# Kernel tuning notes

Measured on AMD Instinct MI355X. Metric: run time of the kernel, lower is better.

The kernel has to match this reference:

```python
import jax, jax.numpy as jnp
import numpy as np

NUM_HEADS = 16
NUM_BUCKETS = 32
MAX_DISTANCE = 128


def _relative_position_bucket(relative_position, num_buckets=NUM_BUCKETS, max_distance=MAX_DISTANCE):
    # bidirectional=True (encoder self-attention)
    nb = num_buckets // 2  # 16
    buckets = (relative_position > 0).astype(jnp.int32) * nb
    rp = jnp.abs(relative_position)
    max_exact = nb // 2  # 8
    is_small = rp < max_exact
    # log-spaced bins for large distances; clamp arg of log to >=1 to avoid log(0)
    rp_f = jnp.maximum(rp, 1).astype(jnp.float32)
    large = max_exact + (
        jnp.log(rp_f / max_exact) / np.log(max_distance / max_exact) * (nb - max_exact)
    ).astype(jnp.int32)
    large = jnp.minimum(large, nb - 1)
    return buckets + jnp.where(is_small, rp, large)


def setup_inputs() -> dict:
    key = jax.random.key(0)
    ks = jax.random.split(key, 6)
    B, L, D = 2, 2048, 1024
    scale = 0.02  # keep activations in a sane range
    return {
        "hidden_states": jax.random.normal(ks[0], (B, L, D), dtype=jnp.float32),
        "Wq": jax.random.normal(ks[1], (D, D), dtype=jnp.float32) * scale,
        "Wk": jax.random.normal(ks[2], (D, D), dtype=jnp.float32) * scale,
        "Wv": jax.random.normal(ks[3], (D, D), dtype=jnp.float32) * scale,
        "Wo": jax.random.normal(ks[4], (D, D), dtype=jnp.float32) * scale,
        "bias_table": jax.random.normal(ks[5], (NUM_BUCKETS, NUM_HEADS), dtype=jnp.float32),
    }


def reference(hidden_states, Wq, Wk, Wv, Wo, bias_table):
    B, L, D = hidden_states.shape
    H = NUM_HEADS
    hd = D // H

    # projections (nn.Linear: y = x @ W.T), split heads -> [B, H, L, hd]
    def proj(x, W):
        return (x @ W.T).reshape(B, L, H, hd).transpose(0, 2, 1, 3)

    q = proj(hidden_states, Wq)
    k = proj(hidden_states, Wk)
    v = proj(hidden_states, Wv)

    # T5 relative position bias: [1, H, L, L]
    ctx = jnp.arange(L)[:, None]
    mem = jnp.arange(L)[None, :]
    buckets = _relative_position_bucket(mem - ctx)  # [L, L]
    position_bias = bias_table[buckets].transpose(2, 0, 1)[None]  # [1, H, L, L]

    # NOTE: T5-style attention has NO 1/sqrt(hd) scaling
    scores = jnp.einsum("bhqd,bhkd->bhqk", q, k) + position_bias
    attn = jax.nn.softmax(scores.astype(jnp.float32), axis=-1).astype(scores.dtype)
    out = jnp.einsum("bhqk,bhkd->bhqd", attn, v)
    out = out.transpose(0, 2, 1, 3).reshape(B, L, D)
    out = out @ Wo.T
    return out, position_bias
```

## Files before the change

kernel.cpp:

```cpp
#include <hip/hip_runtime.h>
#include <cstdint>
#include <cmath>

typedef unsigned short ushort_t;
typedef __bf16 bf16x8 __attribute__((ext_vector_type(8)));
typedef float f32x4 __attribute__((ext_vector_type(4)));
typedef ushort_t us4 __attribute__((ext_vector_type(4)));
typedef ushort_t us8 __attribute__((ext_vector_type(8)));

#define MFMA16(a, b, c) __builtin_amdgcn_mfma_f32_16x16x32_bf16(a, b, c, 0, 0, 0)
#define LOG2E 1.4426950408889634f

__device__ __forceinline__ ushort_t f2bf(float f) {
    uint32_t u = __float_as_uint(f);
    u = u + 0x7fffu + ((u >> 16) & 1u);
    return (ushort_t)(u >> 16);
}

__device__ __forceinline__ void glds16(const ushort_t* g, ushort_t* s) {
    __builtin_amdgcn_global_load_lds(
        (const __attribute__((address_space(1))) void*)(g),
        (__attribute__((address_space(3))) void*)(s), 16, 0, 0);
}

__global__ void cast_all_k(const float* __restrict__ x, const float* __restrict__ wq,
                           const float* __restrict__ wk, const float* __restrict__ wv,
                           const float* __restrict__ wo, ushort_t* __restrict__ xb,
                           ushort_t* __restrict__ wb) {
    int id = blockIdx.x, t = threadIdx.x;
    const float* src;
    ushort_t* dst;
    int idx;
    float scale = 1.0f;
    if (id < 4096) {
        src = x; dst = xb; idx = id * 256 + t;
    } else {
        int r = (id - 4096) >> 10;
        idx = ((id - 4096) & 1023) * 256 + t;
        src = (r == 0) ? wq : (r == 1) ? wk : (r == 2) ? wv : wo;
        dst = wb + (size_t)r * 1048576;
        if (r == 0) scale = LOG2E;
    }
    float4 v = ((const float4*)src)[idx];
    us4 o;
    o.x = f2bf(v.x * scale); o.y = f2bf(v.y * scale);
    o.z = f2bf(v.z * scale); o.w = f2bf(v.w * scale);
    ((us4*)dst)[idx] = o;
}

__global__ void make_lut_k(unsigned char* __restrict__ lut) {
    int idx = blockIdx.x * 256 + threadIdx.x;
    if (idx >= 4095) return;
    int rel = idx - 2047;
    int b = (rel > 0) ? 16 : 0;
    int rp = (rel < 0) ? -rel : rel;
    int add;
    if (rp < 8) {
        add = rp;
    } else {
        float lg = (float)::log((double)rp * 0.125);
        double t = ((double)lg) / 2.772588722239781 * 8.0;
        int large = 8 + (int)t;
        add = (large < 15) ? large : 15;
    }
    lut[idx] = (unsigned char)(b + add);
}

__global__ void write_bias_k(const unsigned char* __restrict__ lut, const float* __restrict__ table,
                             float* __restrict__ out2) {
    int t = blockIdx.x * 256 + threadIdx.x;
    int j4 = t & 511;
    int i = (t >> 9) & 2047;
    int h = t >> 20;
    int base = j4 * 4 - i + 2047;
    float4 v;
    v.x = table[lut[base + 0] * 16 + h];
    v.y = table[lut[base + 1] * 16 + h];
    v.z = table[lut[base + 2] * 16 + h];
    v.w = table[lut[base + 3] * 16 + h];
    ((float4*)out2)[t] = v;
}

template <int MODE>
__global__ __launch_bounds__(256) void gemm_bt_k(const ushort_t* __restrict__ A,
                                                 const ushort_t* __restrict__ B0,
                                                 void* __restrict__ C0,
                                                 int M, int N, int K, long sB, long sC) {
    __shared__ ushort_t As[128 * 64];
    __shared__ ushort_t Bs[128 * 64];
    const int tid = threadIdx.x;
    const int l = tid & 63, w = tid >> 6;
    const int quad = l >> 4, lc = l & 15;
    const int wm = w >> 1, wn = w & 1;
    const int m0 = blockIdx.y * 128, n0 = blockIdx.x * 128;
    const ushort_t* B = B0 + (long)blockIdx.z * sB;

    f32x4 acc[4][4] = {};
    const int rA = l >> 3;
    const int cA = ((l & 7) ^ rA) * 8;

    for (int k0 = 0; k0 < K; k0 += 64) {
#pragma unroll
        for (int t = 0; t < 4; ++t) {
            int row = w * 32 + t * 8;
            glds16(A + (size_t)(m0 + row + rA) * K + k0 + cA, &As[row * 64]);
            glds16(B + (size_t)(n0 + row + rA) * K + k0 + cA, &Bs[row * 64]);
        }
        __syncthreads();
#pragma unroll
        for (int ko = 0; ko < 2; ++ko) {
            const int ch = (((ko * 4 + quad) ^ (lc & 7))) * 8;
            bf16x8 af[4], bfr[4];
#pragma unroll
            for (int mt = 0; mt < 4; ++mt)
                af[mt] = *(const bf16x8*)&As[(wm * 64 + mt * 16 + lc) * 64 + ch];
#pragma unroll
            for (int nt = 0; nt < 4; ++nt)
                bfr[nt] = *(const bf16x8*)&Bs[(wn * 64 + nt * 16 + lc) * 64 + ch];
#pragma unroll
            for (int mt = 0; mt < 4; ++mt)
#pragma unroll
                for (int nt = 0; nt < 4; ++nt)
                    acc[mt][nt] = MFMA16(af[mt], bfr[nt], acc[mt][nt]);
        }
        __syncthreads();
    }
#pragma unroll
    for (int mt = 0; mt < 4; ++mt) {
#pragma unroll
        for (int nt = 0; nt < 4; ++nt) {
            int col = n0 + wn * 64 + nt * 16 + lc;
#pragma unroll
            for (int r = 0; r < 4; ++r) {
                int row = m0 + wm * 64 + mt * 16 + quad * 4 + r;
                if constexpr (MODE == 1) {
                    ((float*)C0)[(size_t)row * N + col] = acc[mt][nt][r];
                } else if constexpr (MODE == 0) {
                    (((ushort_t*)C0) + (long)blockIdx.z * sC)[(size_t)row * N + col] = f2bf(acc[mt][nt][r]);
                } else {
                    ((ushort_t*)C0)[(size_t)(col >> 11) * 2097152 + (size_t)row * 2048 + (col & 2047)] =
                        f2bf(acc[mt][nt][r]);
                }
            }
        }
    }
}

__global__ __launch_bounds__(256, 2) void attn_k(const ushort_t* __restrict__ Qg,
                                                 const ushort_t* __restrict__ Kg,
                                                 const ushort_t* __restrict__ VTg,
                                                 ushort_t* __restrict__ Ctx,
                                                 const unsigned char* __restrict__ lut,
                                                 const float* __restrict__ table) {
    __shared__ ushort_t Ks[128 * 64];
    __shared__ ushort_t VTs[64 * 128];
    __shared__ ushort_t QP[128 * 64];
    __shared__ float biasb[256];

    const int tid = threadIdx.x, l = tid & 63, w = tid >> 6;
    const int quad = l >> 4, lc = l & 15;
    const int id = blockIdx.x;
    const int bh = id & 31, b = bh >> 4, h = bh & 15;
    const int q0 = (id >> 5) * 128;
    const size_t tokbase = (size_t)b * 2048;

    const int rK = l >> 3;
    const int cK = ((l & 7) ^ rK) * 8;
    const int rV = l >> 4;
    const int cVi = l & 15;

#pragma unroll
    for (int t = 0; t < 4; ++t) {
        int row0 = w * 32 + t * 8;
        glds16(Qg + (tokbase + q0 + row0 + rK) * 1024 + h * 64 + cK, &QP[row0 * 64]);
        glds16(Kg + (tokbase + row0 + rK) * 1024 + h * 64 + cK, &Ks[row0 * 64]);
    }
#pragma unroll
    for (int t = 0; t < 4; ++t) {
        int row0 = w * 16 + t * 4;
        int rsw = ((t & 1) * 4 + rV) & 7;
        int csw = (cVi & 8) | ((cVi & 7) ^ rsw);
        glds16(VTg + (size_t)(b * 1024 + h * 64 + row0 + rV) * 2048 + csw * 8, &VTs[row0 * 128]);
    }
    if (tid < 255) biasb[tid] = table[(int)lut[0 - q0 + tid + 1920] * 16 + h] * LOG2E;
    __syncthreads();

    bf16x8 qf[2][2];
#pragma unroll
    for (int nt = 0; nt < 2; ++nt)
#pragma unroll
        for (int ko = 0; ko < 2; ++ko) {
            int row = w * 32 + nt * 16 + lc;
            int ch = ((ko * 4 + quad) ^ (lc & 7)) * 8;
            qf[nt][ko] = *(const bf16x8*)&QP[row * 64 + ch];
        }
    __syncthreads();

    float mstate[2] = {-1e30f, -1e30f};
    float lstate[2] = {0.f, 0.f};
    f32x4 acco[4][2] = {};
    ushort_t* Pw = &QP[w * 1280];
    const int cb0 = quad * 4 - (w * 32 + lc) + 127;
    const int cxor = lc & 3;

    for (int kt = 0; kt < 16; ++kt) {
        const int j0 = kt * 128;
        f32x4 accs[8][2] = {};
#pragma unroll
        for (int ko = 0; ko < 2; ++ko) {
            const int ch = ((ko * 4 + quad) ^ (lc & 7)) * 8;
#pragma unroll
            for (int mt = 0; mt < 8; ++mt) {
                bf16x8 kf = *(const bf16x8*)&Ks[(mt * 16 + lc) * 64 + ch];
                accs[mt][0] = MFMA16(kf, qf[0][ko], accs[mt][0]);
                accs[mt][1] = MFMA16(kf, qf[1][ko], accs[mt][1]);
            }
        }
        f32x4 bv[9];
#pragma unroll
        for (int d = 0; d < 9; ++d)
#pragma unroll
            for (int r = 0; r < 4; ++r) bv[d][r] = biasb[cb0 + (d - 1) * 16 + r];
#pragma unroll
        for (int mt = 0; mt < 8; ++mt)
#pragma unroll
            for (int nt = 0; nt < 2; ++nt)
                accs[mt][nt] += bv[mt - nt + 1];
#pragma unroll
        for (int nt = 0; nt < 2; ++nt) {
            float mx = accs[0][nt][0];
#pragma unroll
            for (int mt = 0; mt < 8; ++mt)
#pragma unroll
                for (int r = 0; r < 4; ++r) mx = fmaxf(mx, accs[mt][nt][r]);
            mx = fmaxf(mx, __shfl_xor(mx, 16, 64));
            mx = fmaxf(mx, __shfl_xor(mx, 32, 64));
            float mo = mstate[nt], mn = fmaxf(mo, mx);
            float alpha = exp2f(mo - mn);
            mstate[nt] = mn;
            float rs = 0.f;
#pragma unroll
            for (int mt = 0; mt < 8; ++mt)
#pragma unroll
                for (int r = 0; r < 4; ++r) {
                    float p = exp2f(accs[mt][nt][r] - mn);
                    accs[mt][nt][r] = p;
                    rs += p;
                }
            rs += __shfl_xor(rs, 16, 64);
            rs += __shfl_xor(rs, 32, 64);
            lstate[nt] = lstate[nt] * alpha + rs;
#pragma unroll
            for (int dt = 0; dt < 4; ++dt) acco[dt][nt] *= alpha;
        }
#pragma unroll
        for (int kk = 0; kk < 4; ++kk) {
#pragma unroll
            for (int half = 0; half < 2; ++half) {
                int mt = kk * 2 + half;
                int c = half * 2 + (quad >> 1);
                int coff = ((c ^ cxor) * 8 + (quad & 1) * 4);
#pragma unroll
                for (int nt = 0; nt < 2; ++nt) {
                    us4 o;
#pragma unroll
                    for (int r = 0; r < 4; ++r) o[r] = f2bf(accs[mt][nt][r]);
                    *(us4*)&Pw[(nt * 16 + lc) * 40 + coff] = o;
                }
            }
            bf16x8 pf[2];
#pragma unroll
            for (int nt = 0; nt < 2; ++nt)
                pf[nt] = *(const bf16x8*)&Pw[(nt * 16 + lc) * 40 + (quad ^ cxor) * 8];
            bf16x8 vf[4];
#pragma unroll
            for (int dt = 0; dt < 4; ++dt) {
                int ch = kk * 4 + quad;
                int chs = ((ch & 8) | ((ch & 7) ^ (lc & 7))) * 8;
                vf[dt] = *(const bf16x8*)&VTs[(dt * 16 + lc) * 128 + chs];
            }
#pragma unroll
            for (int dt = 0; dt < 4; ++dt)
#pragma unroll
                for (int nt = 0; nt < 2; ++nt)
                    acco[dt][nt] = MFMA16(vf[dt], pf[nt], acco[dt][nt]);
        }
        __syncthreads();
        if (kt < 15) {
            const int jn = j0 + 128;
#pragma unroll
            for (int t = 0; t < 4; ++t) {
                int row0 = w * 32 + t * 8;
                glds16(Kg + (tokbase + jn + row0 + rK) * 1024 + h * 64 + cK, &Ks[row0 * 64]);
            }
#pragma unroll
            for (int t = 0; t < 4; ++t) {
                int row0 = w * 16 + t * 4;
                int rsw = ((t & 1) * 4 + rV) & 7;
                int csw = (cVi & 8) | ((cVi & 7) ^ rsw);
                glds16(VTg + (size_t)(b * 1024 + h * 64 + row0 + rV) * 2048 + jn + csw * 8,
                       &VTs[row0 * 128]);
            }
            if (tid < 255) biasb[tid] = table[(int)lut[jn - q0 + tid + 1920] * 16 + h] * LOG2E;
            __syncthreads();
        }
    }
#pragma unroll
    for (int nt = 0; nt < 2; ++nt) {
        float inv = 1.0f / lstate[nt];
        size_t row = tokbase + q0 + w * 32 + nt * 16 + lc;
#pragma unroll
        for (int dt = 0; dt < 4; ++dt) {
            us4 o;
#pragma unroll
            for (int r = 0; r < 4; ++r) o[r] = f2bf(acco[dt][nt][r] * inv);
            *(us4*)&Ctx[row * 1024 + h * 64 + dt * 16 + quad * 4] = o;
        }
    }
}

extern "C" void kernel_launch(void* const* d_in, const int* in_sizes, int n_in,
                              void* d_out, int out_size, void* d_ws, size_t ws_size,
                              hipStream_t stream) {
    const float* hidden = (const float*)d_in[0];
    const float* Wq = (const float*)d_in[1];
    const float* Wk = (const float*)d_in[2];
    const float* Wv = (const float*)d_in[3];
    const float* Wo = (const float*)d_in[4];
    const float* table = (const float*)d_in[5];

    char* ws = (char*)d_ws;
    ushort_t* Xb  = (ushort_t*)(ws);
    ushort_t* Wb  = (ushort_t*)(ws + 8388608);
    ushort_t* Qg  = (ushort_t*)(ws + 16777216);
    ushort_t* Kgp = (ushort_t*)(ws + 25165824);
    ushort_t* VTg = (ushort_t*)(ws + 33554432);
    ushort_t* Ctx = (ushort_t*)(ws + 41943040);
    unsigned char* lutp = (unsigned char*)(ws + 50331648);

    float* out0 = (float*)d_out;
    float* out1 = out0 + 4194304;

    cast_all_k<<<8192, 256, 0, stream>>>(hidden, Wq, Wk, Wv, Wo, Xb, Wb);
    make_lut_k<<<16, 256, 0, stream>>>(lutp);
    write_bias_k<<<65536, 256, 0, stream>>>(lutp, table, out1);

    gemm_bt_k<0><<<dim3(8, 32, 2), 256, 0, stream>>>(Xb, Wb, (void*)Qg,
                                                     4096, 1024, 1024, 1048576, 4194304);
    gemm_bt_k<2><<<dim3(32, 8, 1), 256, 0, stream>>>(Wb + 2097152, Xb, (void*)VTg,
                                                     1024, 4096, 1024, 0, 0);
    attn_k<<<dim3(512), 256, 0, stream>>>(Qg, Kgp, VTg, Ctx, lutp, table);
    gemm_bt_k<1><<<dim3(8, 32, 1), 256, 0, stream>>>(Ctx, Wb + 3145728, (void*)out0,
                                                     4096, 1024, 1024, 0, 0);
}
```

Before: 477.4 us.

## Fuse position-bias output writes into attention and LUT build into cast kernel

Removes the standalone write_bias kernel. The attention kernel now writes the fp32 position-bias tile for its (head, query-block, key-block) with nontemporal stores, using a raw bias buffer kept in shared memory. The LUT construction moves into an extra block of the cast kernel, which saves a launch. It also switches to hardware bf16 conversion and the native exp2, streams the bias vectors instead of holding 9 in registers, and raises the occupancy hint to 3 blocks. The bias tile for head h is computed by both batch blocks, each writing half the columns via b*64, so the 256 MiB of bias writes now compete with attention compute.

```diff
diff --git a/kernel.cpp b/kernel.cpp
--- a/kernel.cpp
+++ b/kernel.cpp
@@ -12,9 +12,9 @@
 #define LOG2E 1.4426950408889634f
 
 __device__ __forceinline__ ushort_t f2bf(float f) {
-    uint32_t u = __float_as_uint(f);
-    u = u + 0x7fffu + ((u >> 16) & 1u);
-    return (ushort_t)(u >> 16);
+    union { __bf16 h; ushort_t u; } cv;
+    cv.h = (__bf16)f;
+    return cv.u;
 }
 
 __device__ __forceinline__ void glds16(const ushort_t* g, ushort_t* s) {
@@ -26,8 +26,26 @@
 __global__ void cast_all_k(const float* __restrict__ x, const float* __restrict__ wq,
                            const float* __restrict__ wk, const float* __restrict__ wv,
                            const float* __restrict__ wo, ushort_t* __restrict__ xb,
-                           ushort_t* __restrict__ wb) {
+                           ushort_t* __restrict__ wb, unsigned char* __restrict__ lut) {
     int id = blockIdx.x, t = threadIdx.x;
+    if (id == 8192) {
+        for (int idx = t; idx < 4095; idx += 256) {
+            int rel = idx - 2047;
+            int bb = (rel > 0) ? 16 : 0;
+            int rp = (rel < 0) ? -rel : rel;
+            int add;
+            if (rp < 8) {
+                add = rp;
+            } else {
+                float lg = (float)::log((double)rp * 0.125);
+                double tt = ((double)lg) / 2.772588722239781 * 8.0;
+                int large = 8 + (int)tt;
+                add = (large < 15) ? large : 15;
+            }
+            lut[idx] = (unsigned char)(bb + add);
+        }
+        return;
+    }
     const float* src;
     ushort_t* dst;
     int idx;
@@ -46,39 +64,6 @@
     o.x = f2bf(v.x * scale); o.y = f2bf(v.y * scale);
     o.z = f2bf(v.z * scale); o.w = f2bf(v.w * scale);
     ((us4*)dst)[idx] = o;
-}
-
-__global__ void make_lut_k(unsigned char* __restrict__ lut) {
-    int idx = blockIdx.x * 256 + threadIdx.x;
-    if (idx >= 4095) return;
-    int rel = idx - 2047;
-    int b = (rel > 0) ? 16 : 0;
-    int rp = (rel < 0) ? -rel : rel;
-    int add;
-    if (rp < 8) {
-        add = rp;
-    } else {
-        float lg = (float)::log((double)rp * 0.125);
-        double t = ((double)lg) / 2.772588722239781 * 8.0;
-        int large = 8 + (int)t;
-        add = (large < 15) ? large : 15;
-    }
-    lut[idx] = (unsigned char)(b + add);
-}
-
-__global__ void write_bias_k(const unsigned char* __restrict__ lut, const float* __restrict__ table,
-                             float* __restrict__ out2) {
-    int t = blockIdx.x * 256 + threadIdx.x;
-    int j4 = t & 511;
-    int i = (t >> 9) & 2047;
-    int h = t >> 20;
-    int base = j4 * 4 - i + 2047;
-    float4 v;
-    v.x = table[lut[base + 0] * 16 + h];
-    v.y = table[lut[base + 1] * 16 + h];
-    v.z = table[lut[base + 2] * 16 + h];
-    v.w = table[lut[base + 3] * 16 + h];
-    ((float4*)out2)[t] = v;
 }
 
 template <int MODE>
@@ -146,16 +131,18 @@
     }
 }
 
-__global__ __launch_bounds__(256, 2) void attn_k(const ushort_t* __restrict__ Qg,
+__global__ __launch_bounds__(256, 3) void attn_k(const ushort_t* __restrict__ Qg,
                                                  const ushort_t* __restrict__ Kg,
                                                  const ushort_t* __restrict__ VTg,
                                                  ushort_t* __restrict__ Ctx,
                                                  const unsigned char* __restrict__ lut,
-                                                 const float* __restrict__ table) {
+                                                 const float* __restrict__ table,
+                                                 float* __restrict__ bias_out) {
     __shared__ ushort_t Ks[128 * 64];
     __shared__ ushort_t VTs[64 * 128];
     __shared__ ushort_t QP[128 * 64];
     __shared__ float biasb[256];
+    __shared__ float biasraw[256];
 
     const int tid = threadIdx.x, l = tid & 63, w = tid >> 6;
     const int quad = l >> 4, lc = l & 15;
@@ -182,7 +169,11 @@
         int csw = (cVi & 8) | ((cVi & 7) ^ rsw);
         glds16(VTg + (size_t)(b * 1024 + h * 64 + row0 + rV) * 2048 + csw * 8, &VTs[row0 * 128]);
     }
-    if (tid < 255) biasb[tid] = table[(int)lut[0 - q0 + tid + 1920] * 16 + h] * LOG2E;
+    if (tid < 255) {
+        float bvv = table[(int)lut[0 - q0 + tid + 1920] * 16 + h];
+        biasraw[tid] = bvv;
+        biasb[tid] = bvv * LOG2E;
+    }
     __syncthreads();
 
     bf16x8 qf[2][2];
@@ -203,6 +194,9 @@
     const int cb0 = quad * 4 - (w * 32 + lc) + 127;
     const int cxor = lc & 3;
 
+    const int bjf = (tid & 15) * 4 + b * 64;
+    const int big = tid >> 4;
+
     for (int kt = 0; kt < 16; ++kt) {
         const int j0 = kt * 128;
         f32x4 accs[8][2] = {};
@@ -216,16 +210,30 @@
                 accs[mt][1] = MFMA16(kf, qf[1][ko], accs[mt][1]);
             }
         }
-        f32x4 bv[9];
-#pragma unroll
-        for (int d = 0; d < 9; ++d)
-#pragma unroll
-            for (int r = 0; r < 4; ++r) bv[d][r] = biasb[cb0 + (d - 1) * 16 + r];
-#pragma unroll
-        for (int mt = 0; mt < 8; ++mt)
-#pragma unroll
-            for (int nt = 0; nt < 2; ++nt)
-                accs[mt][nt] += bv[mt - nt + 1];
+        {
+            float* outp = bias_out + ((size_t)h * 2048 + q0) * 2048 + j0;
+#pragma unroll
+            for (int rr = 0; rr < 8; ++rr) {
+                int il = big + 16 * rr;
+                int d0 = bjf - il + 127;
+                f32x4 v;
+                v[0] = biasraw[d0]; v[1] = biasraw[d0 + 1];
+                v[2] = biasraw[d0 + 2]; v[3] = biasraw[d0 + 3];
+                __builtin_nontemporal_store(v, (f32x4*)(outp + (size_t)il * 2048 + bjf));
+            }
+        }
+        f32x4 bvp;
+#pragma unroll
+        for (int r = 0; r < 4; ++r) bvp[r] = biasb[cb0 - 16 + r];
+#pragma unroll
+        for (int mt = 0; mt < 8; ++mt) {
+            f32x4 bvc;
+#pragma unroll
+            for (int r = 0; r < 4; ++r) bvc[r] = biasb[cb0 + mt * 16 + r];
+            accs[mt][0] += bvc;
+            accs[mt][1] += bvp;
+            bvp = bvc;
+        }
 #pragma unroll
         for (int nt = 0; nt < 2; ++nt) {
             float mx = accs[0][nt][0];
@@ -236,14 +244,14 @@
             mx = fmaxf(mx, __shfl_xor(mx, 16, 64));
             mx = fmaxf(mx, __shfl_xor(mx, 32, 64));
             float mo = mstate[nt], mn = fmaxf(mo, mx);
-            float alpha = exp2f(mo - mn);
+            float alpha = __builtin_amdgcn_exp2f(mo - mn);
             mstate[nt] = mn;
             float rs = 0.f;
 #pragma unroll
             for (int mt = 0; mt < 8; ++mt)
 #pragma unroll
                 for (int r = 0; r < 4; ++r) {
-                    float p = exp2f(accs[mt][nt][r] - mn);
+                    float p = __builtin_amdgcn_exp2f(accs[mt][nt][r] - mn);
                     accs[mt][nt][r] = p;
                     rs += p;
                 }
@@ -301,7 +309,11 @@
                 glds16(VTg + (size_t)(b * 1024 + h * 64 + row0 + rV) * 2048 + jn + csw * 8,
                        &VTs[row0 * 128]);
             }
-            if (tid < 255) biasb[tid] = table[(int)lut[jn - q0 + tid + 1920] * 16 + h] * LOG2E;
+            if (tid < 255) {
+                float bvv = table[(int)lut[jn - q0 + tid + 1920] * 16 + h];
+                biasraw[tid] = bvv;
+                biasb[tid] = bvv * LOG2E;
+            }
             __syncthreads();
         }
     }
@@ -341,15 +353,13 @@
     float* out0 = (float*)d_out;
     float* out1 = out0 + 4194304;
 
-    cast_all_k<<<8192, 256, 0, stream>>>(hidden, Wq, Wk, Wv, Wo, Xb, Wb);
-    make_lut_k<<<16, 256, 0, stream>>>(lutp);
-    write_bias_k<<<65536, 256, 0, stream>>>(lutp, table, out1);
+    cast_all_k<<<8193, 256, 0, stream>>>(hidden, Wq, Wk, Wv, Wo, Xb, Wb, lutp);
 
     gemm_bt_k<0><<<dim3(8, 32, 2), 256, 0, stream>>>(Xb, Wb, (void*)Qg,
                                                      4096, 1024, 1024, 1048576, 4194304);
     gemm_bt_k<2><<<dim3(32, 8, 1), 256, 0, stream>>>(Wb + 2097152, Xb, (void*)VTg,
                                                      1024, 4096, 1024, 0, 0);
-    attn_k<<<dim3(512), 256, 0, stream>>>(Qg, Kgp, VTg, Ctx, lutp, table);
+    attn_k<<<dim3(512), 256, 0, stream>>>(Qg, Kgp, VTg, Ctx, lutp, table, out1);
     gemm_bt_k<1><<<dim3(8, 32, 1), 256, 0, stream>>>(Ctx, Wb + 3145728, (void*)out0,
                                                      4096, 1024, 1024, 0, 0);
 }
```

Result: faster. 461.9 us (-3.2%).
